# Optimization experiments

Measured on AMD Instinct MI355X. Metric: run time of the kernel, lower is better.

Reference implementation:

```python
import jax, jax.numpy as jnp
import numpy as np

L, H, NH, F = 6, 1024, 16, 4096
B, S = 4, 512
D = H // NH
LN_EPS = 1e-12
GELU_C = 0.7978845608028654  # sqrt(2/pi)


def gelu_new(x):
    return 0.5 * x * (1.0 + jnp.tanh(GELU_C * (x + 0.044715 * x * x * x)))


def layer_norm(x, ln):
    # ln: [2, H] -> gamma, beta
    m = jnp.mean(x, axis=-1, keepdims=True)
    v = jnp.mean(jnp.square(x - m), axis=-1, keepdims=True)
    return (x - m) * jax.lax.rsqrt(v + LN_EPS) * ln[0] + ln[1]


def attention(q_in, kv_in, mask, qkv_w, qkv_b):
    # qkv_w: [3, H, H], qkv_b: [3, H]; mask: [B, S_kv] (1 = keep)
    b, s_q, _ = q_in.shape
    s_kv = kv_in.shape[1]
    q = (q_in @ qkv_w[0] + qkv_b[0]).reshape(b, s_q, NH, D)
    k = (kv_in @ qkv_w[1] + qkv_b[1]).reshape(b, s_kv, NH, D)
    v = (kv_in @ qkv_w[2] + qkv_b[2]).reshape(b, s_kv, NH, D)
    scale = 1.0 / (D ** 0.5)
    score = jnp.einsum('bind,bjnd->bnij', q, k) * scale  # [B, NH, Sq, Skv]
    adder = (1.0 - mask.astype(score.dtype))[:, None, None, :] * -10000.0
    prob = jax.nn.softmax(score + adder, axis=-1)
    out = jnp.einsum('bnij,bjnd->bind', prob, v)
    return out.reshape(b, s_q, H)


def _forward(hidden_states, encoder_hidden_states, attention_mask, encoder_attention_mask,
             sa_qkv_w, sa_qkv_b, sa_out_w, sa_out_b, sa_ln,
             ca_qkv_w, ca_qkv_b, ca_out_w, ca_out_b, ca_ln,
             o1_w, o1_b, o1_ln, ffn_w, ffn_b, o2_w, o2_b, o2_ln):
    h = hidden_states
    for i in range(L):
        # self attention + dense/dropout/LN (residual = h)
        self_vec = attention(h, h, attention_mask, sa_qkv_w[i], sa_qkv_b[i])
        attn_out = layer_norm(self_vec @ sa_out_w[i] + sa_out_b[i] + h, sa_ln[i])
        # cross attention + dense/dropout/LN (residual = h, per original code)
        cross_vec = attention(h, encoder_hidden_states, encoder_attention_mask,
                              ca_qkv_w[i], ca_qkv_b[i])
        cross_out = layer_norm(cross_vec @ ca_out_w[i] + ca_out_b[i] + h, ca_ln[i])
        # output_1: dense(attn_out) + cross_out, then LN
        attn_out = layer_norm(attn_out @ o1_w[i] + o1_b[i] + cross_out, o1_ln[i])
        # FFN with gelu_new, output_2: dense(inter) + attn_out, then LN
        inter = gelu_new(attn_out @ ffn_w[i] + ffn_b[i])
        h = layer_norm(inter @ o2_w[i] + o2_b[i] + attn_out, o2_ln[i])
    return h


def setup_inputs() -> dict:
    key = jax.random.key(0)
    ks = jax.random.split(key, 16)
    std = 0.02
    w = lambda k, shape: (jax.random.normal(k, shape, jnp.float32) * std)
    ln_init = jnp.stack([jnp.ones((L, H), jnp.float32), jnp.zeros((L, H), jnp.float32)], axis=1)
    return {
        'hidden_states': jax.random.normal(ks[0], (B, S, H), jnp.float32),
        'encoder_hidden_states': jax.random.normal(ks[1], (B, S, H), jnp.float32),
        'attention_mask': jnp.ones((B, S), jnp.int32),
        'encoder_attention_mask': jnp.ones((B, S), jnp.int32),
        'sa_qkv_w': w(ks[2], (L, 3, H, H)), 'sa_qkv_b': w(ks[3], (L, 3, H)),
        'sa_out_w': w(ks[4], (L, H, H)), 'sa_out_b': w(ks[5], (L, H)), 'sa_ln': ln_init,
        'ca_qkv_w': w(ks[6], (L, 3, H, H)), 'ca_qkv_b': w(ks[7], (L, 3, H)),
        'ca_out_w': w(ks[8], (L, H, H)), 'ca_out_b': w(ks[9], (L, H)), 'ca_ln': ln_init,
        'o1_w': w(ks[10], (L, H, H)), 'o1_b': w(ks[11], (L, H)), 'o1_ln': ln_init,
        'ffn_w': w(ks[12], (L, H, F)), 'ffn_b': w(ks[13], (L, F)),
        'o2_w': w(ks[14], (L, F, H)), 'o2_b': w(ks[15], (L, H)), 'o2_ln': ln_init,
    }


def reference(hidden_states, encoder_hidden_states, attention_mask, encoder_attention_mask,
              sa_qkv_w, sa_qkv_b, sa_out_w, sa_out_b, sa_ln,
              ca_qkv_w, ca_qkv_b, ca_out_w, ca_out_b, ca_ln,
              o1_w, o1_b, o1_ln, ffn_w, ffn_b, o2_w, o2_b, o2_ln):
    return _forward(hidden_states, encoder_hidden_states, attention_mask, encoder_attention_mask,
                    sa_qkv_w, sa_qkv_b, sa_out_w, sa_out_b, sa_ln,
                    ca_qkv_w, ca_qkv_b, ca_out_w, ca_out_b, ca_ln,
                    o1_w, o1_b, o1_ln, ffn_w, ffn_b, o2_w, o2_b, o2_ln)
```

## Files before the change

kernel.cpp:

```cpp
#include <hip/hip_runtime.h>


#define LNUM 6
#define HDIM 1024
#define NHEAD 16
#define DHEAD 64
#define BDIM 4
#define SDIM 512
#define FDIM 4096
#define MROWS (BDIM * SDIM)
#define HSQ (HDIM * HDIM)

typedef __bf16 bf16_t;
typedef bf16_t bf16x8 __attribute__((ext_vector_type(8)));
typedef float f32x4 __attribute__((ext_vector_type(4)));

__device__ __forceinline__ float bf2f(unsigned short u) {
    union { unsigned int i; float f; } x;
    x.i = ((unsigned int)u) << 16;
    return x.f;
}

__device__ __forceinline__ unsigned short f2bf(float f) {
    union { float f; unsigned int i; } u;
    u.f = f;
    unsigned int x = u.i;
    unsigned int lsb = (x >> 16) & 1u;
    x += 0x7fffu + lsb;
    return (unsigned short)(x >> 16);
}

__device__ __forceinline__ void async16(const unsigned short* g, unsigned short* l) {
    __builtin_amdgcn_global_load_lds(
        (const __attribute__((address_space(1))) unsigned int*)g,
        (__attribute__((address_space(3))) unsigned int*)l, 16, 0, 0);
}

template<int N>
__device__ __forceinline__ void s_wait_vmcnt() {
    asm volatile("s_waitcnt vmcnt(%0)" :: "n"(N) : "memory");
}

__device__ __forceinline__ void gemm128_core(
    const unsigned short* __restrict__ Abase,
    const unsigned short* __restrict__ Bbase,
    int K, int kbeg, int kend,
    unsigned short (&As)[3][128][64], unsigned short (&Bs)[3][128][64],
    f32x4 (&acc)[4][2])
{
    const int t = threadIdx.x;
    const int w = t >> 6;
    const int lane = t & 63;
    const int quad = lane >> 4;
    const int cm = lane & 15;
    const int wrow = (w >> 2) * 64;
    const int wcol = (w & 3) * 32;

    const int lrow = lane >> 3;
    const int lcol = ((lane & 7) ^ lrow) * 8;
    const int sw = cm & 7;

    auto stage = [&](int buf, int k0) {
#pragma unroll
        for (int j = 0; j < 2; ++j) {
            int rb = w * 16 + j * 8;
            async16(Abase + (size_t)(rb + lrow) * K + k0 + lcol, &As[buf][rb][0]);
            async16(Bbase + (size_t)(rb + lrow) * K + k0 + lcol, &Bs[buf][rb][0]);
        }
    };

    const int NT = (kend - kbeg) / 64;
    stage(0, kbeg);
    stage(1, kbeg + 64);
    int c0 = 0, c1 = 1, c2 = 2;
    for (int ti = 0; ti < NT; ++ti) {
        if (ti + 2 < NT) {
            stage(c2, kbeg + (ti + 2) * 64);
            s_wait_vmcnt<8>();
        } else if (ti + 1 < NT) {
            s_wait_vmcnt<4>();
        } else {
            s_wait_vmcnt<0>();
        }
        __builtin_amdgcn_s_barrier();
        __builtin_amdgcn_sched_barrier(0);

#pragma unroll
        for (int kk = 0; kk < 64; kk += 32) {
            const int cc = kk >> 3;
            bf16x8 av[4], bv[2];
#pragma unroll
            for (int i = 0; i < 4; ++i)
                av[i] = *(const bf16x8*)&As[c0][wrow + 16 * i + cm][((cc + quad) ^ sw) * 8];
#pragma unroll
            for (int j = 0; j < 2; ++j)
                bv[j] = *(const bf16x8*)&Bs[c0][wcol + 16 * j + cm][((cc + quad) ^ sw) * 8];
#pragma unroll
            for (int i = 0; i < 4; ++i)
#pragma unroll
                for (int j = 0; j < 2; ++j)
                    acc[i][j] = __builtin_amdgcn_mfma_f32_16x16x32_bf16(
                        av[i], bv[j], acc[i][j], 0, 0, 0);
        }

        __builtin_amdgcn_sched_barrier(0);
        __builtin_amdgcn_s_barrier();
        int tmp = c0; c0 = c1; c1 = c2; c2 = tmp;
    }
}

template<bool GELU, bool OUTBF16>
__global__ __launch_bounds__(512) void gemm128(
    const unsigned short* __restrict__ A,
    const unsigned short* __restrict__ BT,
    const float* __restrict__ bias,
    void* __restrict__ Cv,
    int M, int N, int K)
{
    __shared__ unsigned short As[3][128][64];
    __shared__ unsigned short Bs[3][128][64];

    const int row0 = blockIdx.x * 128;
    const int col0 = blockIdx.y * 128;
    const int t = threadIdx.x;
    const int w = t >> 6;
    const int lane = t & 63;
    const int quad = lane >> 4;
    const int cm = lane & 15;
    const int wrow = (w >> 2) * 64;
    const int wcol = (w & 3) * 32;

    f32x4 acc[4][2] = {};
    gemm128_core(A + (size_t)row0 * K, BT + (size_t)col0 * K, K, 0, K, As, Bs, acc);

#pragma unroll
    for (int j = 0; j < 2; ++j) {
        int col = col0 + wcol + 16 * j + cm;
        float bb = bias[col];
#pragma unroll
        for (int i = 0; i < 4; ++i) {
#pragma unroll
            for (int r = 0; r < 4; ++r) {
                int row = row0 + wrow + 16 * i + quad * 4 + r;
                float c = acc[i][j][r] + bb;
                if (GELU) {
                    float u = 0.7978845608028654f * (c + 0.044715f * c * c * c);
                    c = 0.5f * c * (1.0f + tanhf(u));
                }
                if (OUTBF16)
                    ((unsigned short*)Cv)[(size_t)row * N + col] = f2bf(c);
                else
                    ((float*)Cv)[(size_t)row * N + col] = c;
            }
        }
    }
}

__global__ __launch_bounds__(512) void gemm128_qkv6(
    const unsigned short* __restrict__ hA,
    const unsigned short* __restrict__ encA,
    const unsigned short* __restrict__ swq,
    const unsigned short* __restrict__ cwq,
    const float* __restrict__ sb, const float* __restrict__ cb,
    unsigned short* __restrict__ q1, unsigned short* __restrict__ k1,
    unsigned short* __restrict__ v1,
    unsigned short* __restrict__ q2, unsigned short* __restrict__ k2,
    unsigned short* __restrict__ v2,
    int M, int K)
{
    __shared__ unsigned short As[3][128][64];
    __shared__ unsigned short Bs[3][128][64];

    const int row0 = blockIdx.x * 128;
    const int col0 = blockIdx.y * 128;
    const int sec = col0 >> 10;
    const unsigned short* __restrict__ A = (sec <= 3) ? hA : encA;
    const unsigned short* __restrict__ BT =
        (sec < 3) ? swq + (size_t)col0 * K : cwq + (size_t)(col0 - 3072) * K;
    const float* __restrict__ bias = (sec < 3) ? sb + col0 : cb + (col0 - 3072);

    const int t = threadIdx.x;
    const int w = t >> 6;
    const int lane = t & 63;
    const int quad = lane >> 4;
    const int cm = lane & 15;
    const int wrow = (w >> 2) * 64;
    const int wcol = (w & 3) * 32;

    f32x4 acc[4][2] = {};
    gemm128_core(A + (size_t)row0 * K, BT, K, 0, K, As, Bs, acc);

    unsigned short* dst = sec == 0 ? q1 : sec == 1 ? k1 : sec == 2 ? v1
                        : sec == 3 ? q2 : sec == 4 ? k2 : v2;
    const int cbase = col0 & 1023;

#pragma unroll
    for (int j = 0; j < 2; ++j) {
        float bb = bias[wcol + 16 * j + cm];
        int coll = cbase + wcol + 16 * j + cm;
#pragma unroll
        for (int i = 0; i < 4; ++i) {
#pragma unroll
            for (int r = 0; r < 4; ++r) {
                int row = row0 + wrow + 16 * i + quad * 4 + r;
                dst[(size_t)row * HDIM + coll] = f2bf(acc[i][j][r] + bb);
            }
        }
    }
}

__global__ __launch_bounds__(512) void gemm128_out2(
    const unsigned short* __restrict__ A0, const unsigned short* __restrict__ B0,
    const float* __restrict__ b0, float* __restrict__ C0,
    const unsigned short* __restrict__ A1, const unsigned short* __restrict__ B1,
    const float* __restrict__ b1, float* __restrict__ C1,
    int M, int N, int K)
{
    __shared__ unsigned short As[3][128][64];
    __shared__ unsigned short Bs[3][128][64];

    const int z = blockIdx.z;
    const unsigned short* __restrict__ A  = z ? A1 : A0;
    const unsigned short* __restrict__ BT = z ? B1 : B0;
    const float* __restrict__ bias = z ? b1 : b0;
    float* __restrict__ Cv = z ? C1 : C0;

    const int row0 = blockIdx.x * 128;
    const int col0 = blockIdx.y * 128;
    const int t = threadIdx.x;
    const int w = t >> 6;
    const int lane = t & 63;
    const int quad = lane >> 4;
    const int cm = lane & 15;
    const int wrow = (w >> 2) * 64;
    const int wcol = (w & 3) * 32;

    f32x4 acc[4][2] = {};
    gemm128_core(A + (size_t)row0 * K, BT + (size_t)col0 * K, K, 0, K, As, Bs, acc);

#pragma unroll
    for (int j = 0; j < 2; ++j) {
        int col = col0 + wcol + 16 * j + cm;
        float bb = bias[col];
#pragma unroll
        for (int i = 0; i < 4; ++i) {
#pragma unroll
            for (int r = 0; r < 4; ++r) {
                int row = row0 + wrow + 16 * i + quad * 4 + r;
                Cv[(size_t)row * N + col] = acc[i][j][r] + bb;
            }
        }
    }
}

__global__ __launch_bounds__(512) void gemm128_sk2(
    const unsigned short* __restrict__ A,
    const unsigned short* __restrict__ BT,
    const float* __restrict__ bias,
    float* __restrict__ C0, float* __restrict__ C1,
    int M, int N, int K, int Kper)
{
    __shared__ unsigned short As[3][128][64];
    __shared__ unsigned short Bs[3][128][64];

    const int z = blockIdx.z;
    const int kbeg = z * Kper;
    const int row0 = blockIdx.x * 128;
    const int col0 = blockIdx.y * 128;
    const int t = threadIdx.x;
    const int w = t >> 6;
    const int lane = t & 63;
    const int quad = lane >> 4;
    const int cm = lane & 15;
    const int wrow = (w >> 2) * 64;
    const int wcol = (w & 3) * 32;

    f32x4 acc[4][2] = {};
    gemm128_core(A + (size_t)row0 * K, BT + (size_t)col0 * K, K,
                 kbeg, kbeg + Kper, As, Bs, acc);

    float* __restrict__ Cv = z ? C1 : C0;
#pragma unroll
    for (int j = 0; j < 2; ++j) {
        int col = col0 + wcol + 16 * j + cm;
        float bb = z ? 0.0f : bias[col];
#pragma unroll
        for (int i = 0; i < 4; ++i) {
#pragma unroll
            for (int r = 0; r < 4; ++r) {
                int row = row0 + wrow + 16 * i + quad * 4 + r;
                Cv[(size_t)row * N + col] = acc[i][j][r] + bb;
            }
        }
    }
}

__global__ __launch_bounds__(256) void flash_attn(
    const unsigned short* __restrict__ q1, const unsigned short* __restrict__ k1,
    const unsigned short* __restrict__ v1,
    const unsigned short* __restrict__ q2, const unsigned short* __restrict__ k2,
    const unsigned short* __restrict__ v2,
    const int* __restrict__ mask1, const int* __restrict__ mask2,
    unsigned short* __restrict__ ctx1, unsigned short* __restrict__ ctx2)
{
    __shared__ unsigned short Qs[64][64];
    __shared__ unsigned short Ks[64][64];
    __shared__ unsigned short Vs[64][72];
    __shared__ unsigned short Ps[4][16][72];

    const int t = threadIdx.x;
    const int w = t >> 6;
    const int lane = t & 63;
    const int quad = lane >> 4;
    const int cm = lane & 15;
    const int sw = cm & 7;

    const int q0 = blockIdx.x * 64;
    const int h = blockIdx.y;
    const int zz = blockIdx.z;
    const int b = zz & (BDIM - 1);
    const int which = zz >> 2;
    const unsigned short* __restrict__ q = which ? q2 : q1;
    const unsigned short* __restrict__ k = which ? k2 : k1;
    const unsigned short* __restrict__ v = which ? v2 : v1;
    const int* __restrict__ mask = which ? mask2 : mask1;
    unsigned short* __restrict__ ctx = which ? ctx2 : ctx1;

    const size_t rowbase = (size_t)b * SDIM;
    const int hoff = h * DHEAD;

#pragma unroll
    for (int l = 0; l < 2; ++l) {
        int idx = t + l * 256;
        int r = idx >> 3;
        int c = idx & 7;
        *(uint4*)&Qs[r][((c ^ (r & 7)) * 8)] =
            *(const uint4*)(q + (rowbase + q0 + r) * HDIM + hoff + c * 8);
    }

    float m_prev[4] = {-1e30f, -1e30f, -1e30f, -1e30f};
    float l_sum[4] = {0.0f, 0.0f, 0.0f, 0.0f};
    f32x4 oacc[4] = {};

    for (int j0 = 0; j0 < SDIM; j0 += 64) {
        __syncthreads();
#pragma unroll
        for (int l = 0; l < 2; ++l) {
            int idx = t + l * 256;
            int r = idx >> 3;
            int c = idx & 7;
            *(uint4*)&Ks[r][((c ^ (r & 7)) * 8)] =
                *(const uint4*)(k + (rowbase + j0 + r) * HDIM + hoff + c * 8);
        }
#pragma unroll
        for (int l = 0; l < 4; ++l) {
            int idx = t + l * 256;
            int jj = idx >> 4;
            int d0 = (idx & 15) * 4;
            ushort4 vv = *(const ushort4*)(v + (rowbase + j0 + jj) * HDIM + hoff + d0);
            Vs[d0 + 0][jj] = vv.x;
            Vs[d0 + 1][jj] = vv.y;
            Vs[d0 + 2][jj] = vv.z;
            Vs[d0 + 3][jj] = vv.w;
        }
        __syncthreads();

        f32x4 sacc[4] = {};
#pragma unroll
        for (int kk = 0; kk < 64; kk += 32) {
            const int cc = kk >> 3;
            bf16x8 av = *(const bf16x8*)&Qs[w * 16 + cm][((cc + quad) ^ sw) * 8];
#pragma unroll
            for (int j2 = 0; j2 < 4; ++j2) {
                bf16x8 bv = *(const bf16x8*)&Ks[j2 * 16 + cm][((cc + quad) ^ sw) * 8];
                sacc[j2] = __builtin_amdgcn_mfma_f32_16x16x32_bf16(av, bv, sacc[j2], 0, 0, 0);
            }
        }

        float madd[4];
#pragma unroll
        for (int j2 = 0; j2 < 4; ++j2)
            madd[j2] = (1.0f - (float)mask[b * SDIM + j0 + j2 * 16 + cm]) * -10000.0f;

#pragma unroll
        for (int r = 0; r < 4; ++r) {
            float s0 = sacc[0][r] * 0.125f + madd[0];
            float s1 = sacc[1][r] * 0.125f + madd[1];
            float s2 = sacc[2][r] * 0.125f + madd[2];
            float s3 = sacc[3][r] * 0.125f + madd[3];
            float rm = fmaxf(fmaxf(s0, s1), fmaxf(s2, s3));
#pragma unroll
            for (int mo = 1; mo < 16; mo <<= 1)
                rm = fmaxf(rm, __shfl_xor(rm, mo, 64));
            float new_m = fmaxf(m_prev[r], rm);
            float alpha = __expf(m_prev[r] - new_m);
            m_prev[r] = new_m;
            float p0 = __expf(s0 - new_m);
            float p1 = __expf(s1 - new_m);
            float p2 = __expf(s2 - new_m);
            float p3 = __expf(s3 - new_m);
            float rs = p0 + p1 + p2 + p3;
#pragma unroll
            for (int mo = 1; mo < 16; mo <<= 1)
                rs += __shfl_xor(rs, mo, 64);
            l_sum[r] = l_sum[r] * alpha + rs;
#pragma unroll
            for (int d2 = 0; d2 < 4; ++d2)
                oacc[d2][r] *= alpha;
            int prow = quad * 4 + r;
            Ps[w][prow][0 * 16 + cm] = f2bf(p0);
            Ps[w][prow][1 * 16 + cm] = f2bf(p1);
            Ps[w][prow][2 * 16 + cm] = f2bf(p2);
            Ps[w][prow][3 * 16 + cm] = f2bf(p3);
        }

#pragma unroll
        for (int kk = 0; kk < 64; kk += 32) {
            bf16x8 pa = *(const bf16x8*)&Ps[w][cm][kk + quad * 8];
#pragma unroll
            for (int d2 = 0; d2 < 4; ++d2) {
                bf16x8 bv = *(const bf16x8*)&Vs[d2 * 16 + cm][kk + quad * 8];
                oacc[d2] = __builtin_amdgcn_mfma_f32_16x16x32_bf16(pa, bv, oacc[d2], 0, 0, 0);
            }
        }
    }

#pragma unroll
    for (int r = 0; r < 4; ++r) {
        float inv = 1.0f / l_sum[r];
        int row = q0 + w * 16 + quad * 4 + r;
#pragma unroll
        for (int d2 = 0; d2 < 4; ++d2) {
            ctx[(rowbase + row) * HDIM + hoff + d2 * 16 + cm] = f2bf(oacc[d2][r] * inv);
        }
    }
}

__global__ __launch_bounds__(256) void convtrans_all(
    const float* __restrict__ sqkv, const float* __restrict__ sout,
    const float* __restrict__ cqkv, const float* __restrict__ cout,
    const float* __restrict__ o1w,  const float* __restrict__ ffnw,
    const float* __restrict__ o2w,
    unsigned short* __restrict__ dq,  unsigned short* __restrict__ dso,
    unsigned short* __restrict__ dcq, unsigned short* __restrict__ dco,
    unsigned short* __restrict__ do1, unsigned short* __restrict__ dffn,
    unsigned short* __restrict__ do2)
{
    __shared__ unsigned short tile[64][72];
    const int bid = blockIdx.x;
    const float* src;
    unsigned short* dst;
    int K, N, tt;
    if (bid < 2304) {
        int m = bid >> 8;
        tt = bid & 255;
        K = HDIM; N = HDIM;
        if (m < 3)      { src = sqkv + (size_t)m * HSQ;       dst = dq  + (size_t)m * HSQ; }
        else if (m < 6) { src = cqkv + (size_t)(m - 3) * HSQ; dst = dcq + (size_t)(m - 3) * HSQ; }
        else if (m == 6){ src = sout; dst = dso; }
        else if (m == 7){ src = cout; dst = dco; }
        else            { src = o1w;  dst = do1; }
    } else if (bid < 3328) {
        tt = bid - 2304; K = HDIM; N = FDIM; src = ffnw; dst = dffn;
    } else {
        tt = bid - 3328; K = FDIM; N = HDIM; src = o2w; dst = do2;
    }
    const int tn = N >> 6;
    const int n0 = (tt % tn) * 64;
    const int k0 = (tt / tn) * 64;
    const int t = threadIdx.x;
#pragma unroll
    for (int l = 0; l < 4; ++l) {
        int idx = t + l * 256;
        int kk = idx >> 4;
        int nn = (idx & 15) * 4;
        float4 v = *(const float4*)(src + (size_t)(k0 + kk) * N + n0 + nn);
        tile[nn + 0][kk] = f2bf(v.x);
        tile[nn + 1][kk] = f2bf(v.y);
        tile[nn + 2][kk] = f2bf(v.z);
        tile[nn + 3][kk] = f2bf(v.w);
    }
    __syncthreads();
#pragma unroll
    for (int l = 0; l < 2; ++l) {
        int c = t + l * 256;
        int nn = c >> 3;
        int kk = (c & 7) * 8;
        *(uint4*)(dst + (size_t)(n0 + nn) * K + k0 + kk) = *(const uint4*)&tile[nn][kk];
    }
}

__global__ __launch_bounds__(256) void ln2_kernel(
    const float* __restrict__ xa, const float* __restrict__ xb,
    const unsigned short* __restrict__ resid,
    const float* __restrict__ lna, const float* __restrict__ lnb,
    unsigned short* __restrict__ outa, unsigned short* __restrict__ outb)
{
    const int row = blockIdx.x;
    const int z2 = blockIdx.y;
    const float* x = z2 ? xb : xa;
    const float* ln = z2 ? lnb : lna;
    unsigned short* out = z2 ? outb : outa;

    const float* xr = x + (size_t)row * HDIM;
    const unsigned short* rr = resid + (size_t)row * HDIM;
    const int t = threadIdx.x;
    __shared__ float red[4];

    float4 xv = ((const float4*)xr)[t];
    ushort4 rv = ((const ushort4*)rr)[t];
    float z[4];
    z[0] = xv.x + bf2f(rv.x);
    z[1] = xv.y + bf2f(rv.y);
    z[2] = xv.z + bf2f(rv.z);
    z[3] = xv.w + bf2f(rv.w);
    float s = z[0] + z[1] + z[2] + z[3];
#pragma unroll
    for (int off = 32; off > 0; off >>= 1) s += __shfl_down(s, off, 64);
    if ((t & 63) == 0) red[t >> 6] = s;
    __syncthreads();
    s = red[0] + red[1] + red[2] + red[3];
    float mean = s * (1.0f / (float)HDIM);

    float vs = 0.0f;
#pragma unroll
    for (int i = 0; i < 4; ++i) { float d = z[i] - mean; vs += d * d; }
#pragma unroll
    for (int off = 32; off > 0; off >>= 1) vs += __shfl_down(vs, off, 64);
    __syncthreads();
    if ((t & 63) == 0) red[t >> 6] = vs;
    __syncthreads();
    vs = red[0] + red[1] + red[2] + red[3];
    float inv = rsqrtf(vs * (1.0f / (float)HDIM) + 1e-12f);

    const float* g = ln + 4 * t;
    const float* bb = ln + HDIM + 4 * t;
    ushort4 o;
    o.x = f2bf((z[0] - mean) * inv * g[0] + bb[0]);
    o.y = f2bf((z[1] - mean) * inv * g[1] + bb[1]);
    o.z = f2bf((z[2] - mean) * inv * g[2] + bb[2]);
    o.w = f2bf((z[3] - mean) * inv * g[3] + bb[3]);
    ((ushort4*)(out + (size_t)row * HDIM))[t] = o;
}

template<bool OUTF32>
__global__ __launch_bounds__(256) void ln3_kernel(
    const float* __restrict__ xa, const float* __restrict__ xb,
    const unsigned short* __restrict__ resid,
    const float* __restrict__ ln, void* __restrict__ out)
{
    const int row = blockIdx.x;
    const float* xar = xa + (size_t)row * HDIM;
    const float* xbr = xb + (size_t)row * HDIM;
    const unsigned short* rr = resid + (size_t)row * HDIM;
    const int t = threadIdx.x;
    __shared__ float red[4];

    float4 av = ((const float4*)xar)[t];
    float4 bv = ((const float4*)xbr)[t];
    ushort4 rv = ((const ushort4*)rr)[t];
    float z[4];
    z[0] = av.x + bv.x + bf2f(rv.x);
    z[1] = av.y + bv.y + bf2f(rv.y);
    z[2] = av.z + bv.z + bf2f(rv.z);
    z[3] = av.w + bv.w + bf2f(rv.w);
    float s = z[0] + z[1] + z[2] + z[3];
#pragma unroll
    for (int off = 32; off > 0; off >>= 1) s += __shfl_down(s, off, 64);
    if ((t & 63) == 0) red[t >> 6] = s;
    __syncthreads();
    s = red[0] + red[1] + red[2] + red[3];
    float mean = s * (1.0f / (float)HDIM);

    float vs = 0.0f;
#pragma unroll
    for (int i = 0; i < 4; ++i) { float d = z[i] - mean; vs += d * d; }
#pragma unroll
    for (int off = 32; off > 0; off >>= 1) vs += __shfl_down(vs, off, 64);
    __syncthreads();
    if ((t & 63) == 0) red[t >> 6] = vs;
    __syncthreads();
    vs = red[0] + red[1] + red[2] + red[3];
    float inv = rsqrtf(vs * (1.0f / (float)HDIM) + 1e-12f);

    const float* g = ln + 4 * t;
    const float* bb = ln + HDIM + 4 * t;
    if (OUTF32) {
        float4 o;
        o.x = (z[0] - mean) * inv * g[0] + bb[0];
        o.y = (z[1] - mean) * inv * g[1] + bb[1];
        o.z = (z[2] - mean) * inv * g[2] + bb[2];
        o.w = (z[3] - mean) * inv * g[3] + bb[3];
        ((float4*)((float*)out + (size_t)row * HDIM))[t] = o;
    } else {
        ushort4 o;
        o.x = f2bf((z[0] - mean) * inv * g[0] + bb[0]);
        o.y = f2bf((z[1] - mean) * inv * g[1] + bb[1]);
        o.z = f2bf((z[2] - mean) * inv * g[2] + bb[2]);
        o.w = f2bf((z[3] - mean) * inv * g[3] + bb[3]);
        ((ushort4*)((unsigned short*)out + (size_t)row * HDIM))[t] = o;
    }
}

__global__ __launch_bounds__(256) void cvt_bf16_kernel(
    const float* __restrict__ in, unsigned short* __restrict__ out, int n4)
{
    int i = blockIdx.x * 256 + threadIdx.x;
    if (i < n4) {
        float4 v = ((const float4*)in)[i];
        ushort4 o;
        o.x = f2bf(v.x); o.y = f2bf(v.y); o.z = f2bf(v.z); o.w = f2bf(v.w);
        ((ushort4*)out)[i] = o;
    }
}

extern "C" void kernel_launch(void* const* d_in, const int* in_sizes, int n_in,
                              void* d_out, int out_size, void* d_ws, size_t ws_size,
                              hipStream_t stream)
{
    const float* in_hidden = (const float*)d_in[0];
    const float* enc_f     = (const float*)d_in[1];
    const int* attn_mask   = (const int*)d_in[2];
    const int* enc_attn_mask = (const int*)d_in[3];
    const float* sa_qkv_w  = (const float*)d_in[4];
    const float* sa_qkv_b  = (const float*)d_in[5];
    const float* sa_out_w  = (const float*)d_in[6];
    const float* sa_out_b  = (const float*)d_in[7];
    const float* sa_ln     = (const float*)d_in[8];
    const float* ca_qkv_w  = (const float*)d_in[9];
    const float* ca_qkv_b  = (const float*)d_in[10];
    const float* ca_out_w  = (const float*)d_in[11];
    const float* ca_out_b  = (const float*)d_in[12];
    const float* ca_ln     = (const float*)d_in[13];
    const float* o1_w      = (const float*)d_in[14];
    const float* o1_b      = (const float*)d_in[15];
    const float* o1_ln     = (const float*)d_in[16];
    const float* ffn_w     = (const float*)d_in[17];
    const float* ffn_b     = (const float*)d_in[18];
    const float* o2_w      = (const float*)d_in[19];
    const float* o2_b      = (const float*)d_in[20];
    const float* o2_ln     = (const float*)d_in[21];

    const size_t MH  = (size_t)MROWS * HDIM;
    const size_t Hsq = (size_t)HDIM * HDIM;
    const size_t HF  = (size_t)HDIM * FDIM;

    char* p = (char*)d_ws;
    unsigned short* wbf = (unsigned short*)p; p += (9 * Hsq + 2 * HF) * 2;
    float* t2a    = (float*)p; p += MH * 4;
    float* t2b    = (float*)p; p += MH * 4;
    unsigned short* qb     = (unsigned short*)p; p += MH * 2;
    unsigned short* kb     = (unsigned short*)p; p += MH * 2;
    unsigned short* vb     = (unsigned short*)p; p += MH * 2;
    unsigned short* qb2    = (unsigned short*)p; p += MH * 2;
    unsigned short* kb2    = (unsigned short*)p; p += MH * 2;
    unsigned short* vb2    = (unsigned short*)p; p += MH * 2;
    unsigned short* ctx    = (unsigned short*)p; p += MH * 2;
    unsigned short* ctx2   = (unsigned short*)p; p += MH * 2;
    unsigned short* h      = (unsigned short*)p; p += MH * 2;
    unsigned short* enc_bf = (unsigned short*)p; p += MH * 2;
    unsigned short* attn1  = (unsigned short*)p; p += MH * 2;
    unsigned short* crossb = (unsigned short*)p; p += MH * 2;
    unsigned short* attn2  = (unsigned short*)p; p += MH * 2;
    unsigned short* tmp8b  = (unsigned short*)p; p += (size_t)MROWS * FDIM * 2;

    unsigned short* w_saqkv = wbf;
    unsigned short* w_saout = wbf + 3 * Hsq;
    unsigned short* w_caqkv = wbf + 4 * Hsq;
    unsigned short* w_caout = wbf + 7 * Hsq;
    unsigned short* w_o1    = wbf + 8 * Hsq;
    unsigned short* w_ffn   = wbf + 9 * Hsq;
    unsigned short* w_o2    = wbf + 9 * Hsq + HF;

    cvt_bf16_kernel<<<(MH / 4 + 255) / 256, 256, 0, stream>>>(in_hidden, h, MH / 4);
    cvt_bf16_kernel<<<(MH / 4 + 255) / 256, 256, 0, stream>>>(enc_f, enc_bf, MH / 4);

    for (int l = 0; l < LNUM; ++l) {
        convtrans_all<<<4352, 256, 0, stream>>>(
            sa_qkv_w + (size_t)l * 3 * Hsq, sa_out_w + (size_t)l * Hsq,
            ca_qkv_w + (size_t)l * 3 * Hsq, ca_out_w + (size_t)l * Hsq,
            o1_w + (size_t)l * Hsq, ffn_w + (size_t)l * HF, o2_w + (size_t)l * HF,
            w_saqkv, w_saout, w_caqkv, w_caout, w_o1, w_ffn, w_o2);

        gemm128_qkv6<<<dim3(MROWS / 128, 6144 / 128), 512, 0, stream>>>(
            h, enc_bf, w_saqkv, w_caqkv,
            sa_qkv_b + (size_t)l * 3 * HDIM, ca_qkv_b + (size_t)l * 3 * HDIM,
            qb, kb, vb, qb2, kb2, vb2, MROWS, HDIM);

        flash_attn<<<dim3(SDIM / 64, NHEAD, 2 * BDIM), 256, 0, stream>>>(
            qb, kb, vb, qb2, kb2, vb2, attn_mask, enc_attn_mask, ctx, ctx2);

        gemm128_out2<<<dim3(MROWS / 128, HDIM / 128, 2), 512, 0, stream>>>(
            ctx, w_saout, sa_out_b + (size_t)l * HDIM, t2a,
            ctx2, w_caout, ca_out_b + (size_t)l * HDIM, t2b,
            MROWS, HDIM, HDIM);

        ln2_kernel<<<dim3(MROWS, 2), 256, 0, stream>>>(
            t2a, t2b, h, sa_ln + (size_t)l * 2 * HDIM, ca_ln + (size_t)l * 2 * HDIM,
            attn1, crossb);

        gemm128_sk2<<<dim3(MROWS / 128, HDIM / 128, 2), 512, 0, stream>>>(
            attn1, w_o1, o1_b + (size_t)l * HDIM, t2a, t2b, MROWS, HDIM, HDIM, HDIM / 2);
        ln3_kernel<false><<<MROWS, 256, 0, stream>>>(
            t2a, t2b, crossb, o1_ln + (size_t)l * 2 * HDIM, attn2);

        gemm128<true, true><<<dim3(MROWS / 128, FDIM / 128), 512, 0, stream>>>(
            attn2, w_ffn, ffn_b + (size_t)l * FDIM, tmp8b, MROWS, FDIM, HDIM);
        gemm128_sk2<<<dim3(MROWS / 128, HDIM / 128, 2), 512, 0, stream>>>(
            tmp8b, w_o2, o2_b + (size_t)l * HDIM, t2a, t2b, MROWS, HDIM, FDIM, FDIM / 2);
        if (l == LNUM - 1)
            ln3_kernel<true><<<MROWS, 256, 0, stream>>>(
                t2a, t2b, attn2, o2_ln + (size_t)l * 2 * HDIM, (float*)d_out);
        else
            ln3_kernel<false><<<MROWS, 256, 0, stream>>>(
                t2a, t2b, attn2, o2_ln + (size_t)l * 2 * HDIM, h);
    }
}
```

Baseline: 1.780 ms.

## Double-buffer GEMM LDS and batch all-layer weight conversion into one prepass

```diff
diff --git a/kernel.cpp b/kernel.cpp
--- a/kernel.cpp
+++ b/kernel.cpp
@@ -45,7 +45,7 @@
     const unsigned short* __restrict__ Abase,
     const unsigned short* __restrict__ Bbase,
     int K, int kbeg, int kend,
-    unsigned short (&As)[3][128][64], unsigned short (&Bs)[3][128][64],
+    unsigned short (&As)[2][128][64], unsigned short (&Bs)[2][128][64],
     f32x4 (&acc)[4][2])
 {
     const int t = threadIdx.x;
@@ -71,13 +71,10 @@
 
     const int NT = (kend - kbeg) / 64;
     stage(0, kbeg);
-    stage(1, kbeg + 64);
-    int c0 = 0, c1 = 1, c2 = 2;
+    int cur = 0;
     for (int ti = 0; ti < NT; ++ti) {
-        if (ti + 2 < NT) {
-            stage(c2, kbeg + (ti + 2) * 64);
-            s_wait_vmcnt<8>();
-        } else if (ti + 1 < NT) {
+        if (ti + 1 < NT) {
+            stage(cur ^ 1, kbeg + (ti + 1) * 64);
             s_wait_vmcnt<4>();
         } else {
             s_wait_vmcnt<0>();
@@ -91,10 +88,10 @@
             bf16x8 av[4], bv[2];
 #pragma unroll
             for (int i = 0; i < 4; ++i)
-                av[i] = *(const bf16x8*)&As[c0][wrow + 16 * i + cm][((cc + quad) ^ sw) * 8];
+                av[i] = *(const bf16x8*)&As[cur][wrow + 16 * i + cm][((cc + quad) ^ sw) * 8];
 #pragma unroll
             for (int j = 0; j < 2; ++j)
-                bv[j] = *(const bf16x8*)&Bs[c0][wcol + 16 * j + cm][((cc + quad) ^ sw) * 8];
+                bv[j] = *(const bf16x8*)&Bs[cur][wcol + 16 * j + cm][((cc + quad) ^ sw) * 8];
 #pragma unroll
             for (int i = 0; i < 4; ++i)
 #pragma unroll
@@ -105,20 +102,20 @@
 
         __builtin_amdgcn_sched_barrier(0);
         __builtin_amdgcn_s_barrier();
-        int tmp = c0; c0 = c1; c1 = c2; c2 = tmp;
+        cur ^= 1;
     }
 }
 
 template<bool GELU, bool OUTBF16>
-__global__ __launch_bounds__(512) void gemm128(
+__global__ __launch_bounds__(512, 4) void gemm128(
     const unsigned short* __restrict__ A,
     const unsigned short* __restrict__ BT,
     const float* __restrict__ bias,
     void* __restrict__ Cv,
     int M, int N, int K)
 {
-    __shared__ unsigned short As[3][128][64];
-    __shared__ unsigned short Bs[3][128][64];
+    __shared__ unsigned short As[2][128][64];
+    __shared__ unsigned short Bs[2][128][64];
 
     const int row0 = blockIdx.x * 128;
     const int col0 = blockIdx.y * 128;
@@ -156,7 +153,7 @@
     }
 }
 
-__global__ __launch_bounds__(512) void gemm128_qkv6(
+__global__ __launch_bounds__(512, 4) void gemm128_qkv6(
     const unsigned short* __restrict__ hA,
     const unsigned short* __restrict__ encA,
     const unsigned short* __restrict__ swq,
@@ -168,8 +165,8 @@
     unsigned short* __restrict__ v2,
     int M, int K)
 {
-    __shared__ unsigned short As[3][128][64];
-    __shared__ unsigned short Bs[3][128][64];
+    __shared__ unsigned short As[2][128][64];
+    __shared__ unsigned short Bs[2][128][64];
 
     const int row0 = blockIdx.x * 128;
     const int col0 = blockIdx.y * 128;
@@ -209,15 +206,15 @@
     }
 }
 
-__global__ __launch_bounds__(512) void gemm128_out2(
+__global__ __launch_bounds__(512, 4) void gemm128_out2(
     const unsigned short* __restrict__ A0, const unsigned short* __restrict__ B0,
     const float* __restrict__ b0, float* __restrict__ C0,
     const unsigned short* __restrict__ A1, const unsigned short* __restrict__ B1,
     const float* __restrict__ b1, float* __restrict__ C1,
     int M, int N, int K)
 {
-    __shared__ unsigned short As[3][128][64];
-    __shared__ unsigned short Bs[3][128][64];
+    __shared__ unsigned short As[2][128][64];
+    __shared__ unsigned short Bs[2][128][64];
 
     const int z = blockIdx.z;
     const unsigned short* __restrict__ A  = z ? A1 : A0;
@@ -253,15 +250,15 @@
     }
 }
 
-__global__ __launch_bounds__(512) void gemm128_sk2(
+__global__ __launch_bounds__(512, 4) void gemm128_sk2(
     const unsigned short* __restrict__ A,
     const unsigned short* __restrict__ BT,
     const float* __restrict__ bias,
     float* __restrict__ C0, float* __restrict__ C1,
     int M, int N, int K, int Kper)
 {
-    __shared__ unsigned short As[3][128][64];
-    __shared__ unsigned short Bs[3][128][64];
+    __shared__ unsigned short As[2][128][64];
+    __shared__ unsigned short Bs[2][128][64];
 
     const int z = blockIdx.z;
     const int kbeg = z * Kper;
@@ -436,42 +433,71 @@
     }
 }
 
-__global__ __launch_bounds__(256) void convtrans_all(
-    const float* __restrict__ sqkv, const float* __restrict__ sout,
-    const float* __restrict__ cqkv, const float* __restrict__ cout,
-    const float* __restrict__ o1w,  const float* __restrict__ ffnw,
-    const float* __restrict__ o2w,
-    unsigned short* __restrict__ dq,  unsigned short* __restrict__ dso,
-    unsigned short* __restrict__ dcq, unsigned short* __restrict__ dco,
-    unsigned short* __restrict__ do1, unsigned short* __restrict__ dffn,
-    unsigned short* __restrict__ do2)
-{
+#define WSTR (9 * (size_t)HSQ + 2 * (size_t)HDIM * FDIM)
+
+__global__ __launch_bounds__(256) void mega_prepass(
+    const float* __restrict__ sqkv_all, const float* __restrict__ sout_all,
+    const float* __restrict__ cqkv_all, const float* __restrict__ cout_all,
+    const float* __restrict__ o1_all,   const float* __restrict__ ffn_all,
+    const float* __restrict__ o2_all,
+    unsigned short* __restrict__ wbf,
+    const float* __restrict__ hin, const float* __restrict__ encin,
+    unsigned short* __restrict__ hout, unsigned short* __restrict__ encout)
+{
+    const int bid = blockIdx.x;
+    const int t = threadIdx.x;
+
+    if (bid >= 6 * 4352) {
+        int cb = bid - 6 * 4352;
+        const float* src = (cb < 2048) ? hin : encin;
+        unsigned short* dst = (cb < 2048) ? hout : encout;
+        int i = (cb & 2047) * 256 + t;
+        float4 v = ((const float4*)src)[i];
+        ushort4 o;
+        o.x = f2bf(v.x); o.y = f2bf(v.y); o.z = f2bf(v.z); o.w = f2bf(v.w);
+        ((ushort4*)dst)[i] = o;
+        return;
+    }
+
+    const int l = bid / 4352;
+    const int tile_id = bid % 4352;
+    const size_t HF = (size_t)HDIM * FDIM;
+    unsigned short* base = wbf + (size_t)l * WSTR;
+
     __shared__ unsigned short tile[64][72];
-    const int bid = blockIdx.x;
     const float* src;
     unsigned short* dst;
     int K, N, tt;
-    if (bid < 2304) {
-        int m = bid >> 8;
-        tt = bid & 255;
+    if (tile_id < 2304) {
+        int m = tile_id >> 8;
+        tt = tile_id & 255;
         K = HDIM; N = HDIM;
-        if (m < 3)      { src = sqkv + (size_t)m * HSQ;       dst = dq  + (size_t)m * HSQ; }
-        else if (m < 6) { src = cqkv + (size_t)(m - 3) * HSQ; dst = dcq + (size_t)(m - 3) * HSQ; }
-        else if (m == 6){ src = sout; dst = dso; }
-        else if (m == 7){ src = cout; dst = dco; }
-        else            { src = o1w;  dst = do1; }
-    } else if (bid < 3328) {
-        tt = bid - 2304; K = HDIM; N = FDIM; src = ffnw; dst = dffn;
+        if (m < 3) {
+            src = sqkv_all + (size_t)l * 3 * HSQ + (size_t)m * HSQ;
+            dst = base + (size_t)m * HSQ;
+        } else if (m < 6) {
+            src = cqkv_all + (size_t)l * 3 * HSQ + (size_t)(m - 3) * HSQ;
+            dst = base + 4 * (size_t)HSQ + (size_t)(m - 3) * HSQ;
+        } else if (m == 6) {
+            src = sout_all + (size_t)l * HSQ; dst = base + 3 * (size_t)HSQ;
+        } else if (m == 7) {
+            src = cout_all + (size_t)l * HSQ; dst = base + 7 * (size_t)HSQ;
+        } else {
+            src = o1_all + (size_t)l * HSQ;   dst = base + 8 * (size_t)HSQ;
+        }
+    } else if (tile_id < 3328) {
+        tt = tile_id - 2304; K = HDIM; N = FDIM;
+        src = ffn_all + (size_t)l * HF; dst = base + 9 * (size_t)HSQ;
     } else {
-        tt = bid - 3328; K = FDIM; N = HDIM; src = o2w; dst = do2;
+        tt = tile_id - 3328; K = FDIM; N = HDIM;
+        src = o2_all + (size_t)l * HF; dst = base + 9 * (size_t)HSQ + HF;
     }
     const int tn = N >> 6;
     const int n0 = (tt % tn) * 64;
     const int k0 = (tt / tn) * 64;
-    const int t = threadIdx.x;
-#pragma unroll
-    for (int l = 0; l < 4; ++l) {
-        int idx = t + l * 256;
+#pragma unroll
+    for (int ll = 0; ll < 4; ++ll) {
+        int idx = t + ll * 256;
         int kk = idx >> 4;
         int nn = (idx & 15) * 4;
         float4 v = *(const float4*)(src + (size_t)(k0 + kk) * N + n0 + nn);
@@ -482,8 +508,8 @@
     }
     __syncthreads();
 #pragma unroll
-    for (int l = 0; l < 2; ++l) {
-        int c = t + l * 256;
+    for (int ll = 0; ll < 2; ++ll) {
+        int c = t + ll * 256;
         int nn = c >> 3;
         int kk = (c & 7) * 8;
         *(uint4*)(dst + (size_t)(n0 + nn) * K + k0 + kk) = *(const uint4*)&tile[nn][kk];
@@ -599,18 +625,6 @@
         o.z = f2bf((z[2] - mean) * inv * g[2] + bb[2]);
         o.w = f2bf((z[3] - mean) * inv * g[3] + bb[3]);
         ((ushort4*)((unsigned short*)out + (size_t)row * HDIM))[t] = o;
-    }
-}
-
-__global__ __launch_bounds__(256) void cvt_bf16_kernel(
-    const float* __restrict__ in, unsigned short* __restrict__ out, int n4)
-{
-    int i = blockIdx.x * 256 + threadIdx.x;
-    if (i < n4) {
-        float4 v = ((const float4*)in)[i];
-        ushort4 o;
-        o.x = f2bf(v.x); o.y = f2bf(v.y); o.z = f2bf(v.z); o.w = f2bf(v.w);
-        ((ushort4*)out)[i] = o;
     }
 }
 
@@ -646,7 +660,7 @@
     const size_t HF  = (size_t)HDIM * FDIM;
 
     char* p = (char*)d_ws;
-    unsigned short* wbf = (unsigned short*)p; p += (9 * Hsq + 2 * HF) * 2;
+    unsigned short* wbf = (unsigned short*)p; p += 6 * WSTR * 2;
     float* t2a    = (float*)p; p += MH * 4;
     float* t2b    = (float*)p; p += MH * 4;
     unsigned short* qb     = (unsigned short*)p; p += MH * 2;
@@ -664,23 +678,19 @@
     unsigned short* attn2  = (unsigned short*)p; p += MH * 2;
     unsigned short* tmp8b  = (unsigned short*)p; p += (size_t)MROWS * FDIM * 2;
 
-    unsigned short* w_saqkv = wbf;
-    unsigned short* w_saout = wbf + 3 * Hsq;
-    unsigned short* w_caqkv = wbf + 4 * Hsq;
-    unsigned short* w_caout = wbf + 7 * Hsq;
-    unsigned short* w_o1    = wbf + 8 * Hsq;
-    unsigned short* w_ffn   = wbf + 9 * Hsq;
-    unsigned short* w_o2    = wbf + 9 * Hsq + HF;
-
-    cvt_bf16_kernel<<<(MH / 4 + 255) / 256, 256, 0, stream>>>(in_hidden, h, MH / 4);
-    cvt_bf16_kernel<<<(MH / 4 + 255) / 256, 256, 0, stream>>>(enc_f, enc_bf, MH / 4);
+    mega_prepass<<<6 * 4352 + 4096, 256, 0, stream>>>(
+        sa_qkv_w, sa_out_w, ca_qkv_w, ca_out_w, o1_w, ffn_w, o2_w,
+        wbf, in_hidden, enc_f, h, enc_bf);
 
     for (int l = 0; l < LNUM; ++l) {
-        convtrans_all<<<4352, 256, 0, stream>>>(
-            sa_qkv_w + (size_t)l * 3 * Hsq, sa_out_w + (size_t)l * Hsq,
-            ca_qkv_w + (size_t)l * 3 * Hsq, ca_out_w + (size_t)l * Hsq,
-            o1_w + (size_t)l * Hsq, ffn_w + (size_t)l * HF, o2_w + (size_t)l * HF,
-            w_saqkv, w_saout, w_caqkv, w_caout, w_o1, w_ffn, w_o2);
+        unsigned short* base    = wbf + (size_t)l * WSTR;
+        unsigned short* w_saqkv = base;
+        unsigned short* w_saout = base + 3 * Hsq;
+        unsigned short* w_caqkv = base + 4 * Hsq;
+        unsigned short* w_caout = base + 7 * Hsq;
+        unsigned short* w_o1    = base + 8 * Hsq;
+        unsigned short* w_ffn   = base + 9 * Hsq;
+        unsigned short* w_o2    = base + 9 * Hsq + HF;
 
         gemm128_qkv6<<<dim3(MROWS / 128, 6144 / 128), 512, 0, stream>>>(
             h, enc_bf, w_saqkv, w_caqkv,
```

Result: no change. 1.798 ms (+1.0%).
